# Performance work log

Measured on AMD Instinct MI355X. Metric: run time of the kernel, lower is better.

Reference implementation:

```python
import jax, jax.numpy as jnp
import numpy as np

EMBED_DIM = 1024
NUM_HEADS = 16
HEAD_DIM = EMBED_DIM // NUM_HEADS


def setup_inputs() -> dict:
    key = jax.random.key(0)
    ks = jax.random.split(key, 12)
    B, Nq, Nkv, D = 4, 1024, 1024, EMBED_DIM
    s = 1.0 / np.sqrt(D)
    return {
        "query": jax.random.normal(ks[0], (B, Nq, D), jnp.float32),
        "key_value": jax.random.normal(ks[1], (B, Nkv, D), jnp.float32),
        "Wq": jax.random.normal(ks[2], (D, D), jnp.float32) * s,
        "bq": jnp.zeros((D,), jnp.float32),
        "Wk": jax.random.normal(ks[3], (D, D), jnp.float32) * s,
        "bk": jnp.zeros((D,), jnp.float32),
        "Wv": jax.random.normal(ks[4], (D, D), jnp.float32) * s,
        "bv": jnp.zeros((D,), jnp.float32),
        "Wo": jax.random.normal(ks[5], (D, D), jnp.float32) * s,
        "bo": jnp.zeros((D,), jnp.float32),
        "gamma": jnp.ones((D,), jnp.float32),
        "beta": jnp.zeros((D,), jnp.float32),
    }


def reference(query, key_value, Wq, bq, Wk, bk, Wv, bv, Wo, bo, gamma, beta):
    B, Nq, D = query.shape
    Nkv = key_value.shape[1]
    H, Hd = NUM_HEADS, HEAD_DIM
    # projections -> [B, H, N, Hd]
    q = (query @ Wq + bq).reshape(B, Nq, H, Hd).transpose(0, 2, 1, 3)
    k = (key_value @ Wk + bk).reshape(B, Nkv, H, Hd).transpose(0, 2, 1, 3)
    v = (key_value @ Wv + bv).reshape(B, Nkv, H, Hd).transpose(0, 2, 1, 3)
    scores = jnp.einsum("bhqd,bhkd->bhqk", q, k) / jnp.sqrt(jnp.float32(Hd))
    attn = jax.nn.softmax(scores, axis=-1)  # dropout = identity at eval
    out = jnp.einsum("bhqk,bhkd->bhqd", attn, v)
    out = out.transpose(0, 2, 1, 3).reshape(B, Nq, D)
    out = out @ Wo + bo
    # residual + LayerNorm (eps = 1e-5, torch default)
    x = query + out
    mu = jnp.mean(x, axis=-1, keepdims=True)
    var = jnp.mean(jnp.square(x - mu), axis=-1, keepdims=True)
    return (x - mu) / jnp.sqrt(var + 1e-5) * gamma + beta
```

## Files before the change

kernel.cpp:

```cpp
#include <hip/hip_runtime.h>

typedef unsigned short u16;
typedef unsigned int u32;
typedef __attribute__((ext_vector_type(4))) unsigned short u16x4;
typedef __attribute__((ext_vector_type(8))) short short8;
typedef __attribute__((ext_vector_type(4))) float f32x4;

#define MFMA16(a, b, c) __builtin_amdgcn_mfma_f32_16x16x32_bf16(a, b, c, 0, 0, 0)

__device__ __forceinline__ u16 f2bf(float f) {
  unsigned u = __builtin_bit_cast(unsigned, f);
  u += 0x7fffu + ((u >> 16) & 1u);
  return (u16)(u >> 16);
}

__device__ __forceinline__ u32 cvtpk(float lo, float hi) {
  u32 r;
  asm("v_cvt_pk_bf16_f32 %0, %1, %2" : "=v"(r) : "v"(lo), "v"(hi));
  return r;
}

__device__ __forceinline__ float ex2(float x) {
  float r;
  asm("v_exp_f32 %0, %1" : "=v"(r) : "v"(x));
  return r;
}

__device__ __forceinline__ void gl_lds16(const void* g, void* l) {
  __builtin_amdgcn_global_load_lds((const __attribute__((address_space(1))) char*)g,
                                   (__attribute__((address_space(3))) char*)l, 16, 0, 0);
}

__global__ __launch_bounds__(256) void cvt2_k(const float* __restrict__ a,
                                              const float* __restrict__ b,
                                              u16* __restrict__ oa, u16* __restrict__ ob) {
  const int bid = blockIdx.x;
  const float* in = (bid < 4096) ? a : b;
  u16* out = (bid < 4096) ? oa : ob;
  int i = (bid & 4095) * 256 + threadIdx.x;
  float4 v = ((const float4*)in)[i];
  u16x4 o;
  o.x = f2bf(v.x); o.y = f2bf(v.y); o.z = f2bf(v.z); o.w = f2bf(v.w);
  ((u16x4*)out)[i] = o;
}

__global__ __launch_bounds__(256) void wt_k(const float* __restrict__ W0, const float* __restrict__ W1,
                                            const float* __restrict__ W2, const float* __restrict__ W3,
                                            u16* __restrict__ T0, u16* __restrict__ T1,
                                            u16* __restrict__ T2, u16* __restrict__ T3) {
  const float* W; u16* T;
  switch (blockIdx.z) {
    case 0: W = W0; T = T0; break;
    case 1: W = W1; T = T1; break;
    case 2: W = W2; T = T2; break;
    default: W = W3; T = T3; break;
  }
  __shared__ __align__(16) u16 t[64][72];
  const int k0 = blockIdx.y * 64, n0 = blockIdx.x * 64;
  const int tid = threadIdx.x;
  const int r = tid >> 4, c4 = (tid & 15) * 4;
#pragma unroll
  for (int i = 0; i < 4; i++) {
    float4 v = *(const float4*)(W + (k0 + r + i * 16) * 1024 + n0 + c4);
    u16x4 o;
    o.x = f2bf(v.x); o.y = f2bf(v.y); o.z = f2bf(v.z); o.w = f2bf(v.w);
    *(u16x4*)&t[r + i * 16][c4] = o;
  }
  __syncthreads();
#pragma unroll
  for (int i = 0; i < 4; i++) {
    int nr = r + i * 16;
    u16x4 o;
    o.x = t[c4 + 0][nr]; o.y = t[c4 + 1][nr]; o.z = t[c4 + 2][nr]; o.w = t[c4 + 3][nr];
    *(u16x4*)(T + (n0 + nr) * 1024 + k0 + c4) = o;
  }
}

__global__ __launch_bounds__(256, 3) void gemmqkv_k(
    const u16* __restrict__ qbf, const u16* __restrict__ kvbf,
    const u16* __restrict__ Wqt, const u16* __restrict__ Wkt, const u16* __restrict__ Wvt,
    const float* __restrict__ pbq, const float* __restrict__ pbk, const float* __restrict__ pbv,
    u16* __restrict__ Qh, u16* __restrict__ Kh, u16* __restrict__ Vth) {
  const int lin = blockIdx.x;
  const int swz = (lin & 7) * 96 + (lin >> 3);
  const int x = swz & 7, y = (swz >> 3) & 31, z = swz >> 8;

  const u16* A  = (z == 0) ? qbf : kvbf;
  const u16* Bt = (z == 0) ? Wqt : (z == 1 ? Wkt : Wvt);
  const float* bias = (z == 0) ? pbq : (z == 1 ? pbk : pbv);

  __shared__ __align__(16) u16 As[128 * 64];
  __shared__ __align__(16) u16 Bs[128 * 64];
  const int tid = threadIdx.x;
  const int l = tid & 63, w = tid >> 6;
  const int lr = l >> 4, lc = l & 15;
  const int wr = w >> 1, wc = w & 1;
  const int m0 = y * 128, n0 = x * 128;

  f32x4 acc[4][4] = {};

  const int sr = tid >> 2, sc = (tid & 3) * 8;
  const u16* Ag = A + (m0 + sr) * 1024 + sc;
  const u16* Bg = Bt + (n0 + sr) * 1024 + sc;

  for (int k0 = 0; k0 < 1024; k0 += 64) {
    __syncthreads();
    gl_lds16(Ag + k0, As + tid * 8);
    gl_lds16(Ag + 64 * 1024 + k0, As + 2048 + tid * 8);
    gl_lds16(Bg + k0, Bs + tid * 8);
    gl_lds16(Bg + 64 * 1024 + k0, Bs + 2048 + tid * 8);
    gl_lds16(Ag + k0 + 32, As + 4096 + tid * 8);
    gl_lds16(Ag + 64 * 1024 + k0 + 32, As + 6144 + tid * 8);
    gl_lds16(Bg + k0 + 32, Bs + 4096 + tid * 8);
    gl_lds16(Bg + 64 * 1024 + k0 + 32, Bs + 6144 + tid * 8);
    __syncthreads();
    const u16* PA = (z == 2) ? Bs : As;
    const u16* PB = (z == 2) ? As : Bs;
    short8 af[4][2], bf[4][2];
    const int ks8 = lr * 8;
#pragma unroll
    for (int m = 0; m < 4; m++)
#pragma unroll
      for (int h = 0; h < 2; h++)
        af[m][h] = *(const short8*)(PA + h * 4096 + (wr * 64 + m * 16 + lc) * 32 + ks8);
#pragma unroll
    for (int n = 0; n < 4; n++)
#pragma unroll
      for (int h = 0; h < 2; h++)
        bf[n][h] = *(const short8*)(PB + h * 4096 + (wc * 64 + n * 16 + lc) * 32 + ks8);
#pragma unroll
    for (int m = 0; m < 4; m++)
#pragma unroll
      for (int n = 0; n < 4; n++) {
        acc[m][n] = MFMA16(af[m][0], bf[n][0], acc[m][n]);
        acc[m][n] = MFMA16(af[m][1], bf[n][1], acc[m][n]);
      }
  }

  if (z == 2) {
#pragma unroll
    for (int m = 0; m < 4; m++) {
#pragma unroll
      for (int r = 0; r < 4; r++) {
        int ncol = n0 + wr * 64 + m * 16 + lr * 4 + r;
        float bb = bias[ncol];
        int h = ncol >> 6, d = ncol & 63;
#pragma unroll
        for (int n = 0; n < 4; n++) {
          int tok = m0 + wc * 64 + n * 16 + lc;
          Vth[(((tok >> 10) * 16 + h) * 64 + d) * 1024 + (tok & 1023)] =
              f2bf(acc[m][n][r] + bb);
        }
      }
    }
  } else {
    u16* outb = (z == 0) ? Qh : Kh;
    const float scale = (z == 0) ? 0.18033688f : 1.0f;
#pragma unroll
    for (int m = 0; m < 4; m++)
#pragma unroll
      for (int n = 0; n < 4; n++) {
        int ncol = n0 + wc * 64 + n * 16 + lc;
        float bb = bias[ncol];
        int h = ncol >> 6, d = ncol & 63;
#pragma unroll
        for (int r = 0; r < 4; r++) {
          int tok = m0 + wr * 64 + m * 16 + lr * 4 + r;
          outb[(((tok >> 10) * 16 + h) * 1024 + (tok & 1023)) * 64 + d] =
              f2bf((acc[m][n][r] + bb) * scale);
        }
      }
  }
}

__global__ __launch_bounds__(256, 4) void gemmo_k(const u16* __restrict__ A,
                                                  const u16* __restrict__ Bt,
                                                  const float* __restrict__ bias,
                                                  float* __restrict__ outf) {
  const int lin = blockIdx.x;
  const int swz = (lin & 7) * 64 + (lin >> 3);
  const int x = swz & 15, y = swz >> 4;

  __shared__ __align__(16) u16 As[128 * 32];
  __shared__ __align__(16) u16 Bs[64 * 32];
  const int tid = threadIdx.x;
  const int l = tid & 63, w = tid >> 6;
  const int lr = l >> 4, lc = l & 15;
  const int wr = w >> 1, wc = w & 1;
  const int m0 = y * 128, n0 = x * 64;

  f32x4 acc[4][2] = {};
  const int sc = (tid & 3) * 8;
  const u16* Ag = A + (m0 + (tid >> 2)) * 1024 + sc;
  const u16* Bg = Bt + (n0 + (tid >> 2)) * 1024 + sc;

  for (int k0 = 0; k0 < 1024; k0 += 32) {
    __syncthreads();
    gl_lds16(Ag + k0, As + tid * 8);
    gl_lds16(Ag + 64 * 1024 + k0, As + 2048 + tid * 8);
    gl_lds16(Bg + k0, Bs + tid * 8);
    __syncthreads();
    short8 af[4], bf[2];
    const int ks8 = lr * 8;
#pragma unroll
    for (int m = 0; m < 4; m++)
      af[m] = *(const short8*)(As + (wr * 64 + m * 16 + lc) * 32 + ks8);
#pragma unroll
    for (int n = 0; n < 2; n++)
      bf[n] = *(const short8*)(Bs + (wc * 32 + n * 16 + lc) * 32 + ks8);
#pragma unroll
    for (int m = 0; m < 4; m++)
#pragma unroll
      for (int n = 0; n < 2; n++)
        acc[m][n] = MFMA16(af[m], bf[n], acc[m][n]);
  }
#pragma unroll
  for (int m = 0; m < 4; m++)
#pragma unroll
    for (int n = 0; n < 2; n++) {
      int ncol = n0 + wc * 32 + n * 16 + lc;
      float bb = bias[ncol];
#pragma unroll
      for (int r = 0; r < 4; r++) {
        int tok = m0 + wr * 64 + m * 16 + lr * 4 + r;
        outf[tok * 1024 + ncol] = acc[m][n][r] + bb;
      }
    }
}

__global__ __launch_bounds__(256, 2) void attn_k(const u16* __restrict__ Q,
                                                 const u16* __restrict__ K,
                                                 const u16* __restrict__ Vt,
                                                 u16* __restrict__ O) {
  const int bid = blockIdx.x;
  const int xcd = bid & 7, j = bid >> 3;
  const int bh = xcd + 8 * (j & 7);
  const int q0 = (j >> 3) * 128;
  const int tid = threadIdx.x;
  const int w = tid >> 6, l = tid & 63;
  const int lr = l >> 4, lc = l & 15;
  const u16* Qh = Q + bh * (1024 * 64);
  const u16* Kh = K + bh * (1024 * 64);
  const u16* Vh = Vt + bh * (64 * 1024);

  __shared__ __align__(16) u16 Ks[2][64 * 64];
  __shared__ __align__(16) u16 Vs[2][64 * 64];
  __shared__ __align__(16) u32 Plds[4][2][16][32];

  const int st_row = tid >> 3;
  const int st_cb = (tid & 7) * 16;
  const int sw1 = (st_cb ^ ((st_row & 7) << 4)) >> 1;
  const int st_row2 = st_row + 32;
  const int sw2 = (st_cb ^ ((st_row2 & 7) << 4)) >> 1;

  short8 bq[2][2];
#pragma unroll
  for (int g = 0; g < 2; g++)
#pragma unroll
    for (int ks = 0; ks < 2; ks++)
      bq[g][ks] = *(const short8*)(Qh + (q0 + w * 32 + g * 16 + lc) * 64 + ks * 32 + lr * 8);

  f32x4 oacc[2][4] = {};
  float mrun[2] = {-1e30f, -1e30f}, lrun[2] = {0.f, 0.f};

  gl_lds16(Kh + st_row * 64 + sw1, &Ks[0][tid * 8]);
  gl_lds16(Kh + st_row2 * 64 + sw2, &Ks[0][2048 + tid * 8]);
  gl_lds16(Vh + st_row * 1024 + sw1, &Vs[0][tid * 8]);
  gl_lds16(Vh + st_row2 * 1024 + sw2, &Vs[0][2048 + tid * 8]);

  const int xw = (lc & 7) << 2;

  for (int t = 0; t < 16; ++t) {
    const int pb = t & 1;
    if (t < 15) {
      const int kvn = (t + 1) * 64;
      gl_lds16(Kh + (kvn + st_row) * 64 + sw1, &Ks[pb ^ 1][tid * 8]);
      gl_lds16(Kh + (kvn + st_row2) * 64 + sw2, &Ks[pb ^ 1][2048 + tid * 8]);
      gl_lds16(Vh + st_row * 1024 + kvn + sw1, &Vs[pb ^ 1][tid * 8]);
      gl_lds16(Vh + st_row2 * 1024 + kvn + sw2, &Vs[pb ^ 1][2048 + tid * 8]);
      asm volatile("s_waitcnt vmcnt(4)" ::: "memory");
    } else {
      asm volatile("s_waitcnt vmcnt(0)" ::: "memory");
    }
    __builtin_amdgcn_s_barrier();
    asm volatile("" ::: "memory");

    const u16* Kb = Ks[pb];
    const u16* Vb = Vs[pb];

    f32x4 s0[4] = {}, s1[4] = {};
    __builtin_amdgcn_s_setprio(1);
#pragma unroll
    for (int mk = 0; mk < 4; mk++) {
      const int krow = mk * 16 + lc;
      const u16* kp = Kb + krow * 64;
#pragma unroll
      for (int ks = 0; ks < 2; ks++) {
        const int cb = (ks * 64 + lr * 16) ^ ((krow & 7) << 4);
        short8 ak = *(const short8*)(kp + (cb >> 1));
        s0[mk] = MFMA16(ak, bq[0][ks], s0[mk]);
        s1[mk] = MFMA16(ak, bq[1][ks], s1[mk]);
      }
    }
    __builtin_amdgcn_s_setprio(0);

    float mx0, mx1;
    {
      float a = fmaxf(fmaxf(s0[0][0], s0[0][1]), fmaxf(s0[0][2], s0[0][3]));
      float b = fmaxf(fmaxf(s0[1][0], s0[1][1]), fmaxf(s0[1][2], s0[1][3]));
      float c = fmaxf(fmaxf(s0[2][0], s0[2][1]), fmaxf(s0[2][2], s0[2][3]));
      float d = fmaxf(fmaxf(s0[3][0], s0[3][1]), fmaxf(s0[3][2], s0[3][3]));
      mx0 = fmaxf(fmaxf(a, b), fmaxf(c, d));
      float e = fmaxf(fmaxf(s1[0][0], s1[0][1]), fmaxf(s1[0][2], s1[0][3]));
      float f = fmaxf(fmaxf(s1[1][0], s1[1][1]), fmaxf(s1[1][2], s1[1][3]));
      float g2 = fmaxf(fmaxf(s1[2][0], s1[2][1]), fmaxf(s1[2][2], s1[2][3]));
      float h = fmaxf(fmaxf(s1[3][0], s1[3][1]), fmaxf(s1[3][2], s1[3][3]));
      mx1 = fmaxf(fmaxf(e, f), fmaxf(g2, h));
    }
    mx0 = fmaxf(mx0, __shfl_xor(mx0, 16));
    mx0 = fmaxf(mx0, __shfl_xor(mx0, 32));
    mx1 = fmaxf(mx1, __shfl_xor(mx1, 16));
    mx1 = fmaxf(mx1, __shfl_xor(mx1, 32));

    if (!__all(mx0 <= mrun[0] + 8.f && mx1 <= mrun[1] + 8.f)) {
      float mn0 = fmaxf(mrun[0], mx0), mn1 = fmaxf(mrun[1], mx1);
      float al0 = ex2(mrun[0] - mn0), al1 = ex2(mrun[1] - mn1);
      mrun[0] = mn0; mrun[1] = mn1;
      lrun[0] *= al0; lrun[1] *= al1;
      float a0[4], a1[4];
#pragma unroll
      for (int r = 0; r < 4; r++) {
        a0[r] = __shfl(al0, lr * 4 + r);
        a1[r] = __shfl(al1, lr * 4 + r);
      }
#pragma unroll
      for (int nd = 0; nd < 4; nd++)
#pragma unroll
        for (int r = 0; r < 4; r++) {
          oacc[0][nd][r] *= a0[r];
          oacc[1][nd][r] *= a1[r];
        }
    }

    u32* PW0 = &Plds[w][0][lc][0];
    u32* PW1 = &Plds[w][1][lc][0];
#pragma unroll
    for (int mk = 0; mk < 4; mk++)
#pragma unroll
      for (int r = 0; r < 4; r++) {
        s0[mk][r] = ex2(s0[mk][r] - mrun[0]);
        s1[mk][r] = ex2(s1[mk][r] - mrun[1]);
      }
    float ps0, ps1;
    {
      float a = (s0[0][0] + s0[0][1]) + (s0[0][2] + s0[0][3]);
      float b = (s0[1][0] + s0[1][1]) + (s0[1][2] + s0[1][3]);
      float c = (s0[2][0] + s0[2][1]) + (s0[2][2] + s0[2][3]);
      float d = (s0[3][0] + s0[3][1]) + (s0[3][2] + s0[3][3]);
      ps0 = (a + b) + (c + d);
      float e = (s1[0][0] + s1[0][1]) + (s1[0][2] + s1[0][3]);
      float f = (s1[1][0] + s1[1][1]) + (s1[1][2] + s1[1][3]);
      float g2 = (s1[2][0] + s1[2][1]) + (s1[2][2] + s1[2][3]);
      float h = (s1[3][0] + s1[3][1]) + (s1[3][2] + s1[3][3]);
      ps1 = (e + f) + (g2 + h);
    }
    ps0 += __shfl_xor(ps0, 16);
    ps0 += __shfl_xor(ps0, 32);
    ps1 += __shfl_xor(ps1, 16);
    ps1 += __shfl_xor(ps1, 32);
    lrun[0] += ps0;
    lrun[1] += ps1;

#pragma unroll
    for (int mk = 0; mk < 4; mk++)
#pragma unroll
      for (int rr = 0; rr < 2; rr++) {
        PW0[(mk * 8 + lr * 2 + rr) ^ xw] = cvtpk(s0[mk][2 * rr], s0[mk][2 * rr + 1]);
        PW1[(mk * 8 + lr * 2 + rr) ^ xw] = cvtpk(s1[mk][2 * rr], s1[mk][2 * rr + 1]);
      }

    __builtin_amdgcn_s_setprio(1);
#pragma unroll
    for (int ks = 0; ks < 2; ks++) {
      short8 ap0 = *(const short8*)&Plds[w][0][lc][(ks * 16 + lr * 4) ^ xw];
      short8 ap1 = *(const short8*)&Plds[w][1][lc][(ks * 16 + lr * 4) ^ xw];
#pragma unroll
      for (int nd = 0; nd < 4; nd++) {
        const int vrow = nd * 16 + lc;
        const int cb = (ks * 64 + lr * 16) ^ ((vrow & 7) << 4);
        short8 bv = *(const short8*)(Vb + vrow * 64 + (cb >> 1));
        oacc[0][nd] = MFMA16(ap0, bv, oacc[0][nd]);
        oacc[1][nd] = MFMA16(ap1, bv, oacc[1][nd]);
      }
    }
    __builtin_amdgcn_s_setprio(0);

    asm volatile("" ::: "memory");
    __builtin_amdgcn_s_barrier();
  }

  const int b = bh >> 4, h = bh & 15;
#pragma unroll
  for (int g = 0; g < 2; g++) {
    float inv = 1.f / lrun[g];
    float invr[4];
#pragma unroll
    for (int r = 0; r < 4; r++) invr[r] = __shfl(inv, lr * 4 + r);
#pragma unroll
    for (int r = 0; r < 4; r++) {
      int row = b * 1024 + q0 + w * 32 + g * 16 + lr * 4 + r;
#pragma unroll
      for (int nd = 0; nd < 4; nd++)
        O[row * 1024 + h * 64 + nd * 16 + lc] = f2bf(oacc[g][nd][r] * invr[r]);
    }
  }
}

__global__ __launch_bounds__(256) void ln_k(const float* __restrict__ q,
                                            const float* __restrict__ p2,
                                            const float* __restrict__ gamma,
                                            const float* __restrict__ beta,
                                            float* __restrict__ out) {
  const int row = blockIdx.x, tid = threadIdx.x;
  float4 xq = ((const float4*)(q + row * 1024))[tid];
  float4 xp = ((const float4*)(p2 + row * 1024))[tid];
  float4 x = {xq.x + xp.x, xq.y + xp.y, xq.z + xp.z, xq.w + xp.w};
  float s = x.x + x.y + x.z + x.w;
#pragma unroll
  for (int off = 1; off < 64; off <<= 1) s += __shfl_xor(s, off);
  __shared__ float red[8];
  const int w = tid >> 6;
  if ((tid & 63) == 0) red[w] = s;
  __syncthreads();
  float mu = (red[0] + red[1] + red[2] + red[3]) * (1.0f / 1024.0f);
  float4 dx = {x.x - mu, x.y - mu, x.z - mu, x.w - mu};
  float s2 = dx.x * dx.x + dx.y * dx.y + dx.z * dx.z + dx.w * dx.w;
#pragma unroll
  for (int off = 1; off < 64; off <<= 1) s2 += __shfl_xor(s2, off);
  if ((tid & 63) == 0) red[4 + w] = s2;
  __syncthreads();
  float var = (red[4] + red[5] + red[6] + red[7]) * (1.0f / 1024.0f);
  float rs = rsqrtf(var + 1e-5f);
  float4 g = ((const float4*)gamma)[tid];
  float4 bb = ((const float4*)beta)[tid];
  float4 o = {dx.x * rs * g.x + bb.x, dx.y * rs * g.y + bb.y,
              dx.z * rs * g.z + bb.z, dx.w * rs * g.w + bb.w};
  ((float4*)(out + row * 1024))[tid] = o;
}

extern "C" void kernel_launch(void* const* d_in, const int* in_sizes, int n_in,
                              void* d_out, int out_size, void* d_ws, size_t ws_size,
                              hipStream_t stream) {
  const float* query = (const float*)d_in[0];
  const float* kv    = (const float*)d_in[1];
  const float* Wq = (const float*)d_in[2];
  const float* bq = (const float*)d_in[3];
  const float* Wk = (const float*)d_in[4];
  const float* bk = (const float*)d_in[5];
  const float* Wv = (const float*)d_in[6];
  const float* bv = (const float*)d_in[7];
  const float* Wo = (const float*)d_in[8];
  const float* bo = (const float*)d_in[9];
  const float* gamma = (const float*)d_in[10];
  const float* beta  = (const float*)d_in[11];
  float* out = (float*)d_out;

  char* ws = (char*)d_ws;
  const size_t MB = 1u << 20;
  u16* qbf  = (u16*)(ws + 0 * MB);
  u16* kvbf = (u16*)(ws + 8 * MB);
  u16* Wqt  = (u16*)(ws + 16 * MB);
  u16* Wkt  = (u16*)(ws + 18 * MB);
  u16* Wvt  = (u16*)(ws + 20 * MB);
  u16* Wot  = (u16*)(ws + 22 * MB);
  u16* Qh   = (u16*)(ws + 24 * MB);
  u16* Kh   = (u16*)(ws + 32 * MB);
  u16* Vth  = (u16*)(ws + 40 * MB);
  u16* attO = (u16*)(ws + 48 * MB);
  float* p2 = (float*)(ws + 56 * MB);

  cvt2_k<<<dim3(8192), dim3(256), 0, stream>>>(query, kv, qbf, kvbf);
  wt_k<<<dim3(16, 16, 4), dim3(256), 0, stream>>>(Wq, Wk, Wv, Wo, Wqt, Wkt, Wvt, Wot);

  gemmqkv_k<<<dim3(768), dim3(256), 0, stream>>>(qbf, kvbf, Wqt, Wkt, Wvt,
                                                 bq, bk, bv, Qh, Kh, Vth);

  attn_k<<<dim3(512), dim3(256), 0, stream>>>(Qh, Kh, Vth, attO);

  gemmo_k<<<dim3(512), dim3(256), 0, stream>>>(attO, Wot, bo, p2);

  ln_k<<<dim3(4096), dim3(256), 0, stream>>>(query, p2, gamma, beta, out);
}
```

Before: 108.2 us.

## Store output projection in bf16, double gemmo K-step, defer softmax cross-lane reductions

The output-projection GEMM now writes its result as bf16 instead of fp32, and the LayerNorm kernel reads bf16 and widens it. This halves the intermediate write and read traffic at some cost in precision. The GEMM also loads 64-wide K slabs per barrier pair, halving the number of synchronisation rounds. In attention, the row-max shuffles move inside the rare rescale branch, the row-sum shuffles move to the epilogue, and the P tile is written with 64-bit stores. This leaves less cross-lane work in the inner loop, but the skip-rescale test now compares per-lane partial maxima.

```diff
diff --git a/kernel.cpp b/kernel.cpp
--- a/kernel.cpp
+++ b/kernel.cpp
@@ -2,6 +2,7 @@
 
 typedef unsigned short u16;
 typedef unsigned int u32;
+typedef __attribute__((ext_vector_type(2))) unsigned int u32x2;
 typedef __attribute__((ext_vector_type(4))) unsigned short u16x4;
 typedef __attribute__((ext_vector_type(8))) short short8;
 typedef __attribute__((ext_vector_type(4))) float f32x4;
@@ -12,6 +13,10 @@
   unsigned u = __builtin_bit_cast(unsigned, f);
   u += 0x7fffu + ((u >> 16) & 1u);
   return (u16)(u >> 16);
+}
+
+__device__ __forceinline__ float bf2f(u16 b) {
+  return __builtin_bit_cast(float, ((u32)b) << 16);
 }
 
 __device__ __forceinline__ u32 cvtpk(float lo, float hi) {
@@ -176,13 +181,13 @@
 __global__ __launch_bounds__(256, 4) void gemmo_k(const u16* __restrict__ A,
                                                   const u16* __restrict__ Bt,
                                                   const float* __restrict__ bias,
-                                                  float* __restrict__ outf) {
+                                                  u16* __restrict__ outb) {
   const int lin = blockIdx.x;
   const int swz = (lin & 7) * 64 + (lin >> 3);
   const int x = swz & 15, y = swz >> 4;
 
-  __shared__ __align__(16) u16 As[128 * 32];
-  __shared__ __align__(16) u16 Bs[64 * 32];
+  __shared__ __align__(16) u16 As[128 * 64];
+  __shared__ __align__(16) u16 Bs[64 * 64];
   const int tid = threadIdx.x;
   const int l = tid & 63, w = tid >> 6;
   const int lr = l >> 4, lc = l & 15;
@@ -194,25 +199,34 @@
   const u16* Ag = A + (m0 + (tid >> 2)) * 1024 + sc;
   const u16* Bg = Bt + (n0 + (tid >> 2)) * 1024 + sc;
 
-  for (int k0 = 0; k0 < 1024; k0 += 32) {
+  for (int k0 = 0; k0 < 1024; k0 += 64) {
     __syncthreads();
     gl_lds16(Ag + k0, As + tid * 8);
     gl_lds16(Ag + 64 * 1024 + k0, As + 2048 + tid * 8);
     gl_lds16(Bg + k0, Bs + tid * 8);
+    gl_lds16(Ag + k0 + 32, As + 4096 + tid * 8);
+    gl_lds16(Ag + 64 * 1024 + k0 + 32, As + 6144 + tid * 8);
+    gl_lds16(Bg + k0 + 32, Bs + 2048 + tid * 8);
     __syncthreads();
-    short8 af[4], bf[2];
+    short8 af[4][2], bf[2][2];
     const int ks8 = lr * 8;
 #pragma unroll
     for (int m = 0; m < 4; m++)
-      af[m] = *(const short8*)(As + (wr * 64 + m * 16 + lc) * 32 + ks8);
+#pragma unroll
+      for (int h = 0; h < 2; h++)
+        af[m][h] = *(const short8*)(As + h * 4096 + (wr * 64 + m * 16 + lc) * 32 + ks8);
 #pragma unroll
     for (int n = 0; n < 2; n++)
-      bf[n] = *(const short8*)(Bs + (wc * 32 + n * 16 + lc) * 32 + ks8);
+#pragma unroll
+      for (int h = 0; h < 2; h++)
+        bf[n][h] = *(const short8*)(Bs + h * 2048 + (wc * 32 + n * 16 + lc) * 32 + ks8);
 #pragma unroll
     for (int m = 0; m < 4; m++)
 #pragma unroll
-      for (int n = 0; n < 2; n++)
-        acc[m][n] = MFMA16(af[m], bf[n], acc[m][n]);
+      for (int n = 0; n < 2; n++) {
+        acc[m][n] = MFMA16(af[m][0], bf[n][0], acc[m][n]);
+        acc[m][n] = MFMA16(af[m][1], bf[n][1], acc[m][n]);
+      }
   }
 #pragma unroll
   for (int m = 0; m < 4; m++)
@@ -223,7 +237,7 @@
 #pragma unroll
       for (int r = 0; r < 4; r++) {
         int tok = m0 + wr * 64 + m * 16 + lr * 4 + r;
-        outf[tok * 1024 + ncol] = acc[m][n][r] + bb;
+        outb[tok * 1024 + ncol] = f2bf(acc[m][n][r] + bb);
       }
     }
 }
@@ -261,7 +275,8 @@
       bq[g][ks] = *(const short8*)(Qh + (q0 + w * 32 + g * 16 + lc) * 64 + ks * 32 + lr * 8);
 
   f32x4 oacc[2][4] = {};
-  float mrun[2] = {-1e30f, -1e30f}, lrun[2] = {0.f, 0.f};
+  float mrun[2] = {-1e30f, -1e30f};
+  float lrun[2] = {0.f, 0.f};
 
   gl_lds16(Kh + st_row * 64 + sw1, &Ks[0][tid * 8]);
   gl_lds16(Kh + st_row2 * 64 + sw2, &Ks[0][2048 + tid * 8]);
@@ -317,12 +332,12 @@
       float h = fmaxf(fmaxf(s1[3][0], s1[3][1]), fmaxf(s1[3][2], s1[3][3]));
       mx1 = fmaxf(fmaxf(e, f), fmaxf(g2, h));
     }
-    mx0 = fmaxf(mx0, __shfl_xor(mx0, 16));
-    mx0 = fmaxf(mx0, __shfl_xor(mx0, 32));
-    mx1 = fmaxf(mx1, __shfl_xor(mx1, 16));
-    mx1 = fmaxf(mx1, __shfl_xor(mx1, 32));
 
     if (!__all(mx0 <= mrun[0] + 8.f && mx1 <= mrun[1] + 8.f)) {
+      mx0 = fmaxf(mx0, __shfl_xor(mx0, 16));
+      mx0 = fmaxf(mx0, __shfl_xor(mx0, 32));
+      mx1 = fmaxf(mx1, __shfl_xor(mx1, 16));
+      mx1 = fmaxf(mx1, __shfl_xor(mx1, 32));
       float mn0 = fmaxf(mrun[0], mx0), mn1 = fmaxf(mrun[1], mx1);
       float al0 = ex2(mrun[0] - mn0), al1 = ex2(mrun[1] - mn1);
       mrun[0] = mn0; mrun[1] = mn1;
@@ -342,8 +357,6 @@
         }
     }
 
-    u32* PW0 = &Plds[w][0][lc][0];
-    u32* PW1 = &Plds[w][1][lc][0];
 #pragma unroll
     for (int mk = 0; mk < 4; mk++)
 #pragma unroll
@@ -351,33 +364,29 @@
         s0[mk][r] = ex2(s0[mk][r] - mrun[0]);
         s1[mk][r] = ex2(s1[mk][r] - mrun[1]);
       }
-    float ps0, ps1;
     {
       float a = (s0[0][0] + s0[0][1]) + (s0[0][2] + s0[0][3]);
       float b = (s0[1][0] + s0[1][1]) + (s0[1][2] + s0[1][3]);
       float c = (s0[2][0] + s0[2][1]) + (s0[2][2] + s0[2][3]);
       float d = (s0[3][0] + s0[3][1]) + (s0[3][2] + s0[3][3]);
-      ps0 = (a + b) + (c + d);
+      lrun[0] += (a + b) + (c + d);
       float e = (s1[0][0] + s1[0][1]) + (s1[0][2] + s1[0][3]);
       float f = (s1[1][0] + s1[1][1]) + (s1[1][2] + s1[1][3]);
       float g2 = (s1[2][0] + s1[2][1]) + (s1[2][2] + s1[2][3]);
       float h = (s1[3][0] + s1[3][1]) + (s1[3][2] + s1[3][3]);
-      ps1 = (e + f) + (g2 + h);
-    }
-    ps0 += __shfl_xor(ps0, 16);
-    ps0 += __shfl_xor(ps0, 32);
-    ps1 += __shfl_xor(ps1, 16);
-    ps1 += __shfl_xor(ps1, 32);
-    lrun[0] += ps0;
-    lrun[1] += ps1;
-
-#pragma unroll
-    for (int mk = 0; mk < 4; mk++)
-#pragma unroll
-      for (int rr = 0; rr < 2; rr++) {
-        PW0[(mk * 8 + lr * 2 + rr) ^ xw] = cvtpk(s0[mk][2 * rr], s0[mk][2 * rr + 1]);
-        PW1[(mk * 8 + lr * 2 + rr) ^ xw] = cvtpk(s1[mk][2 * rr], s1[mk][2 * rr + 1]);
-      }
+      lrun[1] += (e + f) + (g2 + h);
+    }
+
+    u32* PW0 = &Plds[w][0][lc][0];
+    u32* PW1 = &Plds[w][1][lc][0];
+#pragma unroll
+    for (int mk = 0; mk < 4; mk++) {
+      const int idx = (mk * 8 + lr * 2) ^ xw;
+      u32x2 p0 = {cvtpk(s0[mk][0], s0[mk][1]), cvtpk(s0[mk][2], s0[mk][3])};
+      u32x2 p1 = {cvtpk(s1[mk][0], s1[mk][1]), cvtpk(s1[mk][2], s1[mk][3])};
+      *(u32x2*)&PW0[idx] = p0;
+      *(u32x2*)&PW1[idx] = p1;
+    }
 
     __builtin_amdgcn_s_setprio(1);
 #pragma unroll
@@ -402,7 +411,10 @@
   const int b = bh >> 4, h = bh & 15;
 #pragma unroll
   for (int g = 0; g < 2; g++) {
-    float inv = 1.f / lrun[g];
+    float lsum = lrun[g];
+    lsum += __shfl_xor(lsum, 16);
+    lsum += __shfl_xor(lsum, 32);
+    float inv = 1.f / lsum;
     float invr[4];
 #pragma unroll
     for (int r = 0; r < 4; r++) invr[r] = __shfl(inv, lr * 4 + r);
@@ -417,14 +429,15 @@
 }
 
 __global__ __launch_bounds__(256) void ln_k(const float* __restrict__ q,
-                                            const float* __restrict__ p2,
+                                            const u16* __restrict__ p2,
                                             const float* __restrict__ gamma,
                                             const float* __restrict__ beta,
                                             float* __restrict__ out) {
   const int row = blockIdx.x, tid = threadIdx.x;
   float4 xq = ((const float4*)(q + row * 1024))[tid];
-  float4 xp = ((const float4*)(p2 + row * 1024))[tid];
-  float4 x = {xq.x + xp.x, xq.y + xp.y, xq.z + xp.z, xq.w + xp.w};
+  u16x4 xpb = ((const u16x4*)(p2 + row * 1024))[tid];
+  float4 x = {xq.x + bf2f(xpb.x), xq.y + bf2f(xpb.y),
+              xq.z + bf2f(xpb.z), xq.w + bf2f(xpb.w)};
   float s = x.x + x.y + x.z + x.w;
 #pragma unroll
   for (int off = 1; off < 64; off <<= 1) s += __shfl_xor(s, off);
@@ -477,7 +490,7 @@
   u16* Kh   = (u16*)(ws + 32 * MB);
   u16* Vth  = (u16*)(ws + 40 * MB);
   u16* attO = (u16*)(ws + 48 * MB);
-  float* p2 = (float*)(ws + 56 * MB);
+  u16* p2b  = (u16*)(ws + 56 * MB);
 
   cvt2_k<<<dim3(8192), dim3(256), 0, stream>>>(query, kv, qbf, kvbf);
   wt_k<<<dim3(16, 16, 4), dim3(256), 0, stream>>>(Wq, Wk, Wv, Wo, Wqt, Wkt, Wvt, Wot);
@@ -487,7 +500,7 @@
 
   attn_k<<<dim3(512), dim3(256), 0, stream>>>(Qh, Kh, Vth, attO);
 
-  gemmo_k<<<dim3(512), dim3(256), 0, stream>>>(attO, Wot, bo, p2);
-
-  ln_k<<<dim3(4096), dim3(256), 0, stream>>>(query, p2, gamma, beta, out);
-}
+  gemmo_k<<<dim3(512), dim3(256), 0, stream>>>(attO, Wot, bo, p2b);
+
+  ln_k<<<dim3(4096), dim3(256), 0, stream>>>(query, p2b, gamma, beta, out);
+}
```

New measurement: 101.5 us. -6.2%, faster.
